# Kernel tuning notes

Measured on AMD Instinct MI355X. Metric: run time of the kernel, lower is better.

The kernel has to match this reference:

```python
import jax, jax.numpy as jnp
import numpy as np

N_E = 4096
E_DIM = 256


def setup_inputs() -> dict:
    key = jax.random.key(0)
    k1, k2 = jax.random.split(key)
    z = jax.random.normal(k1, (32, 2048, E_DIM), dtype=jnp.float32)
    # nn.Embedding weight initialized uniform(-1/n_e, 1/n_e)
    codebook = jax.random.uniform(k2, (N_E, E_DIM), dtype=jnp.float32,
                                  minval=-1.0 / N_E, maxval=1.0 / N_E)
    return {"z": z, "codebook": codebook}


def reference(z, codebook):
    # z: [B, T, e_dim], codebook: [n_e, e_dim]
    z_flat = z.reshape(-1, z.shape[-1])                      # [N, d]
    # squared euclidean distance: ||z||^2 + ||e||^2 - 2 z.e^T
    d = (jnp.sum(z_flat ** 2, axis=1, keepdims=True)
         + jnp.sum(codebook ** 2, axis=1)
         - 2.0 * jnp.einsum('nd,kd->nk', z_flat, codebook))  # [N, n_e]
    idx = jnp.argmin(d, axis=1)                              # [N]
    z_q = codebook[idx].reshape(z.shape)                     # [B, T, d]
    return z_q
```

## Files before the change

kernel.cpp:

```cpp
#include <hip/hip_runtime.h>
#include <hip/hip_fp16.h>
#include <cfloat>
#include <climits>

#define D     256
#define NE    4096
#define MT    64
#define NSPLITB 8
#define DELTA     1.5e-4f
#define CAND_CAP  131072

typedef _Float16 f16x8 __attribute__((ext_vector_type(8)));
typedef __attribute__((ext_vector_type(4))) float f32x4;

#define SYNC(n) do { \
    asm volatile("s_waitcnt vmcnt(" #n ")\n\ts_barrier" ::: "memory"); \
    __builtin_amdgcn_sched_barrier(0); \
} while (0)

__device__ __forceinline__ float np_block128_sq(const float* __restrict__ p) {
    float r[8];
    #pragma unroll
    for (int j = 0; j < 8; ++j) r[j] = __fmul_rn(p[j], p[j]);
    #pragma unroll
    for (int i = 8; i < 128; i += 8)
        #pragma unroll
        for (int j = 0; j < 8; ++j) r[j] = __fadd_rn(r[j], __fmul_rn(p[i + j], p[i + j]));
    return __fadd_rn(__fadd_rn(__fadd_rn(r[0], r[1]), __fadd_rn(r[2], r[3])),
                     __fadd_rn(__fadd_rn(r[4], r[5]), __fadd_rn(r[6], r[7])));
}
__device__ __forceinline__ float np_sumsq256(const float* __restrict__ p) {
    return __fadd_rn(np_block128_sq(p), np_block128_sq(p + 128));
}
__device__ __forceinline__ float np_einsum_dot256(const float* __restrict__ zr,
                                                  const float* __restrict__ er) {
    float v0 = 0.f, v1 = 0.f, v2 = 0.f, v3 = 0.f;
    for (int t = 0; t < 256; t += 16) {
        float4 a0 = *(const float4*)(zr + t);
        float4 a1 = *(const float4*)(zr + t + 4);
        float4 a2 = *(const float4*)(zr + t + 8);
        float4 a3 = *(const float4*)(zr + t + 12);
        float4 b0 = *(const float4*)(er + t);
        float4 b1 = *(const float4*)(er + t + 4);
        float4 b2 = *(const float4*)(er + t + 8);
        float4 b3 = *(const float4*)(er + t + 12);
        v0 = __fadd_rn(v0, __fmul_rn(a3.x, b3.x));
        v1 = __fadd_rn(v1, __fmul_rn(a3.y, b3.y));
        v2 = __fadd_rn(v2, __fmul_rn(a3.z, b3.z));
        v3 = __fadd_rn(v3, __fmul_rn(a3.w, b3.w));
        v0 = __fadd_rn(v0, __fmul_rn(a2.x, b2.x));
        v1 = __fadd_rn(v1, __fmul_rn(a2.y, b2.y));
        v2 = __fadd_rn(v2, __fmul_rn(a2.z, b2.z));
        v3 = __fadd_rn(v3, __fmul_rn(a2.w, b2.w));
        v0 = __fadd_rn(v0, __fmul_rn(a1.x, b1.x));
        v1 = __fadd_rn(v1, __fmul_rn(a1.y, b1.y));
        v2 = __fadd_rn(v2, __fmul_rn(a1.z, b1.z));
        v3 = __fadd_rn(v3, __fmul_rn(a1.w, b1.w));
        v0 = __fadd_rn(v0, __fmul_rn(a0.x, b0.x));
        v1 = __fadd_rn(v1, __fmul_rn(a0.y, b0.y));
        v2 = __fadd_rn(v2, __fmul_rn(a0.z, b0.z));
        v3 = __fadd_rn(v3, __fmul_rn(a0.w, b0.w));
    }
    return __fadd_rn(__fadd_rn(v0, v1), __fadd_rn(v2, v3));
}

__global__ void bnp_kernel(const float* __restrict__ cb, float* __restrict__ Bnp,
                           unsigned short* __restrict__ Bnpb) {
    int k = blockIdx.x * 256 + threadIdx.x;
    if (k < NE) {
        float s = np_sumsq256(cb + (size_t)k * D);
        Bnp[k] = s;
        unsigned u = __float_as_uint(s);
        Bnpb[k] = (unsigned short)((u + 0x7FFFu + ((u >> 16) & 1u)) >> 16);
    }
}

__global__ void tof16_kernel(const float* __restrict__ x,
                             unsigned short* __restrict__ y, float scale, int n4) {
    int t = blockIdx.x * 256 + threadIdx.x;
    if (t >= n4) return;
    float4 v = *(const float4*)(x + (size_t)t * 4);
    ushort4 o;
    o.x = __half_as_ushort(__float2half_rn(v.x * scale));
    o.y = __half_as_ushort(__float2half_rn(v.y * scale));
    o.z = __half_as_ushort(__float2half_rn(v.z * scale));
    o.w = __half_as_ushort(__float2half_rn(v.w * scale));
    *(ushort4*)(y + (size_t)t * 4) = o;
}

__device__ __forceinline__ void gload_lds16(const void* g, void* l) {
    __builtin_amdgcn_global_load_lds(
        (const __attribute__((address_space(1))) unsigned int*)g,
        (__attribute__((address_space(3))) unsigned int*)l, 16, 0, 0);
}

__global__ __launch_bounds__(256, 3)
void stageA_f16(const float* __restrict__ z,
                const unsigned short* __restrict__ cb2,
                const unsigned short* __restrict__ Bnpb, int* __restrict__ idxArr,
                float* __restrict__ rowMin, unsigned long long* __restrict__ rowKey,
                int* __restrict__ flagCnt, int* __restrict__ flagList) {
    __shared__ unsigned char lds[8192 + 4 * 8192];
    unsigned short* BnpL = (unsigned short*)lds;
    unsigned short* Bt = (unsigned short*)(lds + 8192);

    const int tid  = threadIdx.x;
    const int wid  = tid >> 6;
    const int lane = tid & 63;
    const int ln   = lane & 15;
    const int qd   = lane >> 4;
    const int wm   = wid & 1;
    const int wn   = wid >> 1;
    const int R0   = blockIdx.x * MT;

    #pragma unroll
    for (int i = 0; i < 2; ++i) {
        int j = tid + 256 * i;
        *(uint4*)(BnpL + j * 8) = *(const uint4*)(Bnpb + j * 8);
    }

    f16x8 fa[8][2];
    {
        const float* za = z + (size_t)(R0 + wm * 32 + ln) * 256 + qd * 8;
        #pragma unroll
        for (int kc = 0; kc < 8; ++kc)
            #pragma unroll
            for (int mt = 0; mt < 2; ++mt) {
                const float* p = za + mt * 16 * 256 + kc * 32;
                float4 a = *(const float4*)p, b = *(const float4*)(p + 4);
                f16x8 h;
                h[0] = (_Float16)a.x; h[1] = (_Float16)a.y;
                h[2] = (_Float16)a.z; h[3] = (_Float16)a.w;
                h[4] = (_Float16)b.x; h[5] = (_Float16)b.y;
                h[6] = (_Float16)b.z; h[7] = (_Float16)b.w;
                fa[kc][mt] = h;
            }
    }

    const int cA  = wid * 32 + (lane >> 2);
    const int sgA = (lane & 3) ^ ((cA >> 1) & 3);
    const unsigned short* srcA = cb2 + cA * 256 + sgA * 8;
    unsigned short* dstW = Bt + wid * 1024;
    const int boffs = ((wn * 64 + ln) << 6) + ((qd ^ ((ln >> 1) & 3)) << 4);
    const unsigned char* btb = (const unsigned char*)Bt;

    float best1[8], best2[8];
    int   bidx[8];
    #pragma unroll
    for (int i = 0; i < 8; ++i) { best1[i] = FLT_MAX; best2[i] = FLT_MAX; bidx[i] = 0; }

    #pragma unroll
    for (int s = 0; s < 3; ++s) {
        gload_lds16(srcA + s * 32, dstW + s * 4096);
        gload_lds16(srcA + s * 32 + 4096, dstW + s * 4096 + 512);
    }
    __syncthreads();

    for (int ct = 0; ct < 31; ++ct) {
        f32x4 acc[2][4];
        #pragma unroll
        for (int i = 0; i < 2; ++i)
            #pragma unroll
            for (int j = 0; j < 4; ++j) acc[i][j] = (f32x4){0.f, 0.f, 0.f, 0.f};

        #pragma unroll
        for (int kc = 0; kc < 8; ++kc) {
            SYNC(4);
            {
                const int s3k = kc + 3;
                int off = (ct + (s3k >> 3)) * 32768 + (s3k & 7) * 32;
                unsigned short* d = dstW + ((s3k & 3) << 12);
                gload_lds16(srcA + off, d);
                gload_lds16(srcA + off + 4096, d + 512);
            }
            f16x8 fb[4];
            #pragma unroll
            for (int nt = 0; nt < 4; ++nt)
                fb[nt] = *(const f16x8*)(btb + ((kc & 3) << 13) + boffs + nt * 1024);
            __builtin_amdgcn_s_setprio(1);
            #pragma unroll
            for (int mt = 0; mt < 2; ++mt)
                #pragma unroll
                for (int nt = 0; nt < 4; ++nt)
                    acc[mt][nt] = __builtin_amdgcn_mfma_f32_16x16x32_f16(
                        fa[kc][mt], fb[nt], acc[mt][nt], 0, 0, 0);
            __builtin_amdgcn_s_setprio(0);

            if (kc == 7) {
                const int C0 = ct * 128;
                #pragma unroll
                for (int nt = 0; nt < 4; ++nt) {
                    int col = C0 + wn * 64 + nt * 16 + ln;
                    float bn = __uint_as_float(((unsigned)BnpL[col]) << 16);
                    #pragma unroll
                    for (int mt = 0; mt < 2; ++mt) {
                        f32x4 a = acc[mt][nt];
                        #pragma unroll
                        for (int r = 0; r < 4; ++r) {
                            float s = fmaf(-4.8828125e-4f, a[r], bn);
                            int ii = mt * 4 + r;
                            bool lt = s < best1[ii];
                            best2[ii] = __builtin_amdgcn_fmed3f(best1[ii], best2[ii], s);
                            bidx[ii]  = lt ? col : bidx[ii];
                            best1[ii] = fminf(best1[ii], s);
                        }
                    }
                }
            }
        }
    }
    {
        const int ct = 31;
        f32x4 acc[2][4];
        #pragma unroll
        for (int i = 0; i < 2; ++i)
            #pragma unroll
            for (int j = 0; j < 4; ++j) acc[i][j] = (f32x4){0.f, 0.f, 0.f, 0.f};

        #pragma unroll
        for (int kc = 0; kc < 8; ++kc) {
            if (kc <= 5) { SYNC(4); } else if (kc == 6) { SYNC(2); } else { SYNC(0); }
            if (kc <= 4) {
                const int s3k = kc + 3;
                int off = ct * 32768 + (s3k & 7) * 32;
                unsigned short* d = dstW + ((s3k & 3) << 12);
                gload_lds16(srcA + off, d);
                gload_lds16(srcA + off + 4096, d + 512);
            }
            f16x8 fb[4];
            #pragma unroll
            for (int nt = 0; nt < 4; ++nt)
                fb[nt] = *(const f16x8*)(btb + ((kc & 3) << 13) + boffs + nt * 1024);
            __builtin_amdgcn_s_setprio(1);
            #pragma unroll
            for (int mt = 0; mt < 2; ++mt)
                #pragma unroll
                for (int nt = 0; nt < 4; ++nt)
                    acc[mt][nt] = __builtin_amdgcn_mfma_f32_16x16x32_f16(
                        fa[kc][mt], fb[nt], acc[mt][nt], 0, 0, 0);
            __builtin_amdgcn_s_setprio(0);

            if (kc == 7) {
                const int C0 = ct * 128;
                #pragma unroll
                for (int nt = 0; nt < 4; ++nt) {
                    int col = C0 + wn * 64 + nt * 16 + ln;
                    float bn = __uint_as_float(((unsigned)BnpL[col]) << 16);
                    #pragma unroll
                    for (int mt = 0; mt < 2; ++mt) {
                        f32x4 a = acc[mt][nt];
                        #pragma unroll
                        for (int r = 0; r < 4; ++r) {
                            float s = fmaf(-4.8828125e-4f, a[r], bn);
                            int ii = mt * 4 + r;
                            bool lt = s < best1[ii];
                            best2[ii] = __builtin_amdgcn_fmed3f(best1[ii], best2[ii], s);
                            bidx[ii]  = lt ? col : bidx[ii];
                            best1[ii] = fminf(best1[ii], s);
                        }
                    }
                }
            }
        }
    }

    #pragma unroll
    for (int mask = 1; mask < 16; mask <<= 1) {
        #pragma unroll
        for (int ii = 0; ii < 8; ++ii) {
            float c1 = __shfl_xor(best1[ii], mask);
            float c2 = __shfl_xor(best2[ii], mask);
            int   ci = __shfl_xor(bidx[ii], mask);
            if (c1 < best1[ii] || (c1 == best1[ii] && ci < bidx[ii])) {
                best2[ii] = fminf(best1[ii], c2);
                best1[ii] = c1; bidx[ii] = ci;
            } else {
                best2[ii] = fminf(best2[ii], c1);
            }
        }
    }
    __syncthreads();
    float* mb1 = (float*)lds;
    float* mb2 = mb1 + 128;
    int*   mix = (int*)(mb2 + 128);
    if (ln == 0) {
        #pragma unroll
        for (int mt = 0; mt < 2; ++mt)
            #pragma unroll
            for (int r = 0; r < 4; ++r) {
                int row = wm * 32 + mt * 16 + qd * 4 + r;
                mb1[row * 2 + wn] = best1[mt * 4 + r];
                mb2[row * 2 + wn] = best2[mt * 4 + r];
                mix[row * 2 + wn] = bidx[mt * 4 + r];
            }
    }
    __syncthreads();
    if (tid < MT) {
        int r = tid;
        float b1 = mb1[r * 2], b2v = mb2[r * 2]; int ix = mix[r * 2];
        float c1 = mb1[r * 2 + 1], c2 = mb2[r * 2 + 1]; int ci = mix[r * 2 + 1];
        if (c1 < b1 || (c1 == b1 && ci < ix)) { b2v = fminf(b1, c2); b1 = c1; ix = ci; }
        else b2v = fminf(b2v, c1);
        idxArr[R0 + r] = ix;
        rowMin[R0 + r] = b1;
        rowKey[R0 + r] = ~0ULL;
        if (b2v - b1 <= DELTA) {
            int p = atomicAdd(flagCnt, 1);
            flagList[p] = R0 + r;
        }
    }
}

__global__ __launch_bounds__(256, 2)
void stageB_f16(const float* __restrict__ z,
                const unsigned short* __restrict__ cb2,
                const float* __restrict__ Bnp, const float* __restrict__ rowMin,
                const int* __restrict__ flagCnt, const int* __restrict__ flagList,
                int* __restrict__ candCnt, unsigned int* __restrict__ candList) {
    __shared__ unsigned char lds[4 * 8192 + 512];
    unsigned short* Bt = (unsigned short*)lds;
    int*   frow   = (int*)(lds + 32768);
    float* rmin_l = (float*)(lds + 32768 + 256);

    const int nf = *flagCnt;
    const int R0 = blockIdx.x * MT;
    if (R0 >= nf) return;
    const int m = min(MT, nf - R0);

    const int tid  = threadIdx.x;
    const int wid  = tid >> 6;
    const int lane = tid & 63;
    const int ln   = lane & 15;
    const int qd   = lane >> 4;
    const int wn   = wid;
    const int ktBeg = blockIdx.y * (NE / NSPLITB);

    if (tid < MT) {
        int fr = flagList[R0 + min(tid, m - 1)];
        frow[tid] = fr;
        rmin_l[tid] = rowMin[fr];
    }
    __syncthreads();

    float rmv[16];
    #pragma unroll
    for (int mt = 0; mt < 4; ++mt)
        #pragma unroll
        for (int r = 0; r < 4; ++r)
            rmv[mt * 4 + r] = rmin_l[mt * 16 + qd * 4 + r];

    float bnv[4][2];
    #pragma unroll
    for (int ct = 0; ct < 4; ++ct)
        #pragma unroll
        for (int nt = 0; nt < 2; ++nt)
            bnv[ct][nt] = Bnp[ktBeg + ct * 128 + wn * 32 + nt * 16 + ln];

    f16x8 fa[8][4];
    {
        int rA[4];
        #pragma unroll
        for (int mt = 0; mt < 4; ++mt) rA[mt] = frow[mt * 16 + ln];
        #pragma unroll
        for (int kc = 0; kc < 8; ++kc)
            #pragma unroll
            for (int mt = 0; mt < 4; ++mt) {
                const float* p = z + (size_t)rA[mt] * 256 + kc * 32 + qd * 8;
                float4 a = *(const float4*)p, b = *(const float4*)(p + 4);
                f16x8 h;
                h[0] = (_Float16)a.x; h[1] = (_Float16)a.y;
                h[2] = (_Float16)a.z; h[3] = (_Float16)a.w;
                h[4] = (_Float16)b.x; h[5] = (_Float16)b.y;
                h[6] = (_Float16)b.z; h[7] = (_Float16)b.w;
                fa[kc][mt] = h;
            }
    }

    const int cA  = wid * 32 + (lane >> 2);
    const int sgA = (lane & 3) ^ ((cA >> 1) & 3);
    const unsigned short* srcA = cb2 + (size_t)(ktBeg + cA) * 256 + sgA * 8;
    unsigned short* dstW = Bt + wid * 1024;
    const int boffs = ((wn * 32 + ln) << 6) + ((qd ^ ((ln >> 1) & 3)) << 4);
    const unsigned char* btb = (const unsigned char*)Bt;

    #pragma unroll
    for (int s = 0; s < 3; ++s) {
        gload_lds16(srcA + s * 32, dstW + s * 4096);
        gload_lds16(srcA + s * 32 + 4096, dstW + s * 4096 + 512);
    }
    __syncthreads();

    unsigned long long hm0 = 0, hm1 = 0;

    #pragma unroll
    for (int ct = 0; ct < 4; ++ct) {
        f32x4 acc[4][2];
        #pragma unroll
        for (int i = 0; i < 4; ++i)
            #pragma unroll
            for (int j = 0; j < 2; ++j) acc[i][j] = (f32x4){0.f, 0.f, 0.f, 0.f};

        #pragma unroll
        for (int kc = 0; kc < 8; ++kc) {
            const int s = ct * 8 + kc;
            if (s <= 29) { SYNC(4); } else if (s == 30) { SYNC(2); } else { SYNC(0); }
            if (s <= 28) {
                const int s3 = s + 3;
                int off = (s3 >> 3) * 32768 + (s3 & 7) * 32;
                unsigned short* d = dstW + ((s3 & 3) << 12);
                gload_lds16(srcA + off, d);
                gload_lds16(srcA + off + 4096, d + 512);
            }
            f16x8 fb[2];
            #pragma unroll
            for (int nt = 0; nt < 2; ++nt)
                fb[nt] = *(const f16x8*)(btb + ((s & 3) << 13) + boffs + nt * 1024);
            __builtin_amdgcn_s_setprio(1);
            #pragma unroll
            for (int mt = 0; mt < 4; ++mt)
                #pragma unroll
                for (int nt = 0; nt < 2; ++nt)
                    acc[mt][nt] = __builtin_amdgcn_mfma_f32_16x16x32_f16(
                        fa[kc][mt], fb[nt], acc[mt][nt], 0, 0, 0);
            __builtin_amdgcn_s_setprio(0);

            if (kc == 7) {
                #pragma unroll
                for (int nt = 0; nt < 2; ++nt)
                    #pragma unroll
                    for (int mt = 0; mt < 4; ++mt) {
                        f32x4 a = acc[mt][nt];
                        #pragma unroll
                        for (int r = 0; r < 4; ++r) {
                            float sc = fmaf(-4.8828125e-4f, a[r], bnv[ct][nt]);
                            if (sc <= rmv[mt * 4 + r] + DELTA) {
                                unsigned long long bit =
                                    1ull << (((ct & 1) << 5) | (nt << 4) | (mt << 2) | r);
                                if (ct < 2) hm0 |= bit; else hm1 |= bit;
                            }
                        }
                    }
            }
        }
    }

    #pragma unroll
    for (int h = 0; h < 2; ++h) {
        unsigned long long hm = h ? hm1 : hm0;
        while (hm) {
            int b = __builtin_ctzll(hm);
            hm &= hm - 1;
            int ctb = h * 2 + (b >> 5);
            int ntb = (b >> 4) & 1, mtb = (b >> 2) & 3, rb = b & 3;
            int col = ktBeg + ctb * 128 + wn * 32 + ntb * 16 + ln;
            int row = frow[mtb * 16 + qd * 4 + rb];
            int p = atomicAdd(candCnt, 1);
            if (p < CAND_CAP)
                candList[p] = ((unsigned)row << 12) | (unsigned)col;
        }
    }
}

__global__ void stageC(const float* __restrict__ z, const float* __restrict__ cb,
                       const float* __restrict__ Bnp,
                       const int* __restrict__ candCnt,
                       const unsigned int* __restrict__ candList,
                       unsigned long long* __restrict__ rowKey) {
    int c = blockIdx.x * 256 + threadIdx.x;
    int n = min(*candCnt, CAND_CAP);
    if (c >= n) return;
    unsigned e = candList[c];
    int r = (int)(e >> 12);
    int k = (int)(e & 4095u);
    float Anp = np_sumsq256(z + (size_t)r * D);
    float C   = np_einsum_dot256(z + (size_t)r * D, cb + (size_t)k * D);
    float AB  = __fadd_rn(Anp, Bnp[k]);
    float s   = __fsub_rn(AB, __fadd_rn(C, C));
    unsigned long long key = ((unsigned long long)__float_as_uint(s) << 32) | (unsigned)k;
    atomicMin(rowKey + r, key);
}

__global__ void gather_kernel(const float* __restrict__ cb,
                              const int* __restrict__ idxArr,
                              const unsigned long long* __restrict__ rowKey,
                              float* __restrict__ out) {
    int r = blockIdx.x * 4 + (threadIdx.x >> 6);
    int l = threadIdx.x & 63;
    unsigned long long kv = rowKey[r];
    int ix = (kv != ~0ULL) ? (int)(kv & 0xFFFFFFFFull) : idxArr[r];
    *(float4*)(out + (size_t)r * D + l * 4) =
        *(const float4*)(cb + (size_t)ix * D + l * 4);
}

extern "C" void kernel_launch(void* const* d_in, const int* in_sizes, int n_in,
                              void* d_out, int out_size, void* d_ws, size_t ws_size,
                              hipStream_t stream) {
    const float* z  = (const float*)d_in[0];
    const float* cb = (const float*)d_in[1];
    float* out = (float*)d_out;
    const int nRows = in_sizes[0] / D;

    char* w = (char*)d_ws;
    unsigned short* cb2 = (unsigned short*)w;
    unsigned long long* rowKey = (unsigned long long*)(w + 2097152);
    int*   idxArr   = (int*)  (w + 2621440);
    float* rowMin   = (float*)(w + 2883584);
    int*   flagList = (int*)  (w + 3145728);
    float* Bnp      = (float*)(w + 3407872);
    unsigned short* Bnpb = (unsigned short*)(w + 3424256);
    unsigned int* candList = (unsigned int*)(w + 3432448);
    int*   flagCnt  = (int*)  (w + 3956736);
    int*   candCnt  = flagCnt + 1;

    hipMemsetAsync(flagCnt, 0, 8, stream);
    bnp_kernel<<<NE / 256, 256, 0, stream>>>(cb, Bnp, Bnpb);
    tof16_kernel<<<NE * D / 4 / 256, 256, 0, stream>>>(cb, cb2, 4096.0f, NE * D / 4);
    stageA_f16<<<nRows / MT, 256, 0, stream>>>(z, cb2, Bnpb, idxArr, rowMin,
                                               rowKey, flagCnt, flagList);
    stageB_f16<<<dim3(nRows / MT, NSPLITB), 256, 0, stream>>>(z, cb2, Bnp, rowMin,
                                                              flagCnt, flagList,
                                                              candCnt, candList);
    stageC<<<CAND_CAP / 256, 256, 0, stream>>>(z, cb, Bnp, candCnt, candList, rowKey);
    gather_kernel<<<nRows / 4, 256, 0, stream>>>(cb, idxArr, rowKey, out);
}
```

Before: 438.4 us.

## Shrink stage A row tile and give each wave its own codebook slice

Stage A now processes 32 rows per block instead of 64. Each of the four waves owns a private 32-column slice of the codebook tile, which it streams into its own LDS region. This replaces the block-wide barriers in the K loop with per-wave vmcnt waits only, and the final reduction merges four per-wave candidates instead of two. The cost is that every codebook byte is now loaded for half as many rows, which doubles codebook traffic through L2, and each wave issues fewer MFMAs per B fragment load.

```diff
diff --git a/kernel.cpp b/kernel.cpp
--- a/kernel.cpp
+++ b/kernel.cpp
@@ -5,13 +5,19 @@
 
 #define D     256
 #define NE    4096
-#define MT    64
+#define MTA   32
+#define MTB   64
 #define NSPLITB 8
 #define DELTA     1.5e-4f
 #define CAND_CAP  131072
 
 typedef _Float16 f16x8 __attribute__((ext_vector_type(8)));
 typedef __attribute__((ext_vector_type(4))) float f32x4;
+
+#define WAITV(n) do { \
+    asm volatile("s_waitcnt vmcnt(" #n ")" ::: "memory"); \
+    __builtin_amdgcn_sched_barrier(0); \
+} while (0)
 
 #define SYNC(n) do { \
     asm volatile("s_waitcnt vmcnt(" #n ")\n\ts_barrier" ::: "memory"); \
@@ -102,16 +108,13 @@
                 int* __restrict__ flagCnt, int* __restrict__ flagList) {
     __shared__ unsigned char lds[8192 + 4 * 8192];
     unsigned short* BnpL = (unsigned short*)lds;
-    unsigned short* Bt = (unsigned short*)(lds + 8192);
 
     const int tid  = threadIdx.x;
     const int wid  = tid >> 6;
     const int lane = tid & 63;
     const int ln   = lane & 15;
     const int qd   = lane >> 4;
-    const int wm   = wid & 1;
-    const int wn   = wid >> 1;
-    const int R0   = blockIdx.x * MT;
+    const int R0   = blockIdx.x * MTA;
 
     #pragma unroll
     for (int i = 0; i < 2; ++i) {
@@ -121,7 +124,7 @@
 
     f16x8 fa[8][2];
     {
-        const float* za = z + (size_t)(R0 + wm * 32 + ln) * 256 + qd * 8;
+        const float* za = z + (size_t)(R0 + ln) * 256 + qd * 8;
         #pragma unroll
         for (int kc = 0; kc < 8; ++kc)
             #pragma unroll
@@ -137,60 +140,61 @@
             }
     }
 
-    const int cA  = wid * 32 + (lane >> 2);
-    const int sgA = (lane & 3) ^ ((cA >> 1) & 3);
-    const unsigned short* srcA = cb2 + cA * 256 + sgA * 8;
-    unsigned short* dstW = Bt + wid * 1024;
-    const int boffs = ((wn * 64 + ln) << 6) + ((qd ^ ((ln >> 1) & 3)) << 4);
-    const unsigned char* btb = (const unsigned char*)Bt;
+    const int cL  = lane >> 2;
+    const int sgA = (lane & 3) ^ ((cL >> 1) & 3);
+    const unsigned short* srcA = cb2 + (wid * 32 + cL) * 256 + sgA * 8;
+    unsigned short* dstW = (unsigned short*)(lds + 8192) + wid * 4096;
+    const unsigned char* btb = lds + 8192 + wid * 8192;
+    const int boffs = (ln << 6) + ((qd ^ ((ln >> 1) & 3)) << 4);
 
     float best1[8], best2[8];
     int   bidx[8];
     #pragma unroll
     for (int i = 0; i < 8; ++i) { best1[i] = FLT_MAX; best2[i] = FLT_MAX; bidx[i] = 0; }
 
+    __syncthreads();
+
     #pragma unroll
     for (int s = 0; s < 3; ++s) {
-        gload_lds16(srcA + s * 32, dstW + s * 4096);
-        gload_lds16(srcA + s * 32 + 4096, dstW + s * 4096 + 512);
-    }
-    __syncthreads();
+        gload_lds16(srcA + s * 32, dstW + s * 1024);
+        gload_lds16(srcA + s * 32 + 4096, dstW + s * 1024 + 512);
+    }
 
     for (int ct = 0; ct < 31; ++ct) {
-        f32x4 acc[2][4];
+        f32x4 acc[2][2];
         #pragma unroll
         for (int i = 0; i < 2; ++i)
             #pragma unroll
-            for (int j = 0; j < 4; ++j) acc[i][j] = (f32x4){0.f, 0.f, 0.f, 0.f};
+            for (int j = 0; j < 2; ++j) acc[i][j] = (f32x4){0.f, 0.f, 0.f, 0.f};
 
         #pragma unroll
         for (int kc = 0; kc < 8; ++kc) {
-            SYNC(4);
+            WAITV(4);
             {
                 const int s3k = kc + 3;
                 int off = (ct + (s3k >> 3)) * 32768 + (s3k & 7) * 32;
-                unsigned short* d = dstW + ((s3k & 3) << 12);
+                unsigned short* d = dstW + ((s3k & 3) << 10);
                 gload_lds16(srcA + off, d);
                 gload_lds16(srcA + off + 4096, d + 512);
             }
-            f16x8 fb[4];
-            #pragma unroll
-            for (int nt = 0; nt < 4; ++nt)
-                fb[nt] = *(const f16x8*)(btb + ((kc & 3) << 13) + boffs + nt * 1024);
+            f16x8 fb[2];
+            #pragma unroll
+            for (int nt = 0; nt < 2; ++nt)
+                fb[nt] = *(const f16x8*)(btb + ((kc & 3) << 11) + boffs + nt * 1024);
             __builtin_amdgcn_s_setprio(1);
             #pragma unroll
             for (int mt = 0; mt < 2; ++mt)
                 #pragma unroll
-                for (int nt = 0; nt < 4; ++nt)
+                for (int nt = 0; nt < 2; ++nt)
                     acc[mt][nt] = __builtin_amdgcn_mfma_f32_16x16x32_f16(
                         fa[kc][mt], fb[nt], acc[mt][nt], 0, 0, 0);
             __builtin_amdgcn_s_setprio(0);
 
             if (kc == 7) {
-                const int C0 = ct * 128;
+                const int C0 = ct * 128 + wid * 32;
                 #pragma unroll
-                for (int nt = 0; nt < 4; ++nt) {
-                    int col = C0 + wn * 64 + nt * 16 + ln;
+                for (int nt = 0; nt < 2; ++nt) {
+                    int col = C0 + nt * 16 + ln;
                     float bn = __uint_as_float(((unsigned)BnpL[col]) << 16);
                     #pragma unroll
                     for (int mt = 0; mt < 2; ++mt) {
@@ -211,40 +215,40 @@
     }
     {
         const int ct = 31;
-        f32x4 acc[2][4];
+        f32x4 acc[2][2];
         #pragma unroll
         for (int i = 0; i < 2; ++i)
             #pragma unroll
-            for (int j = 0; j < 4; ++j) acc[i][j] = (f32x4){0.f, 0.f, 0.f, 0.f};
+            for (int j = 0; j < 2; ++j) acc[i][j] = (f32x4){0.f, 0.f, 0.f, 0.f};
 
         #pragma unroll
         for (int kc = 0; kc < 8; ++kc) {
-            if (kc <= 5) { SYNC(4); } else if (kc == 6) { SYNC(2); } else { SYNC(0); }
+            if (kc <= 5) { WAITV(4); } else if (kc == 6) { WAITV(2); } else { WAITV(0); }
             if (kc <= 4) {
                 const int s3k = kc + 3;
                 int off = ct * 32768 + (s3k & 7) * 32;
-                unsigned short* d = dstW + ((s3k & 3) << 12);
+                unsigned short* d = dstW + ((s3k & 3) << 10);
                 gload_lds16(srcA + off, d);
                 gload_lds16(srcA + off + 4096, d + 512);
             }
-            f16x8 fb[4];
-            #pragma unroll
-            for (int nt = 0; nt < 4; ++nt)
-                fb[nt] = *(const f16x8*)(btb + ((kc & 3) << 13) + boffs + nt * 1024);
+            f16x8 fb[2];
+            #pragma unroll
+            for (int nt = 0; nt < 2; ++nt)
+                fb[nt] = *(const f16x8*)(btb + ((kc & 3) << 11) + boffs + nt * 1024);
             __builtin_amdgcn_s_setprio(1);
             #pragma unroll
             for (int mt = 0; mt < 2; ++mt)
                 #pragma unroll
-                for (int nt = 0; nt < 4; ++nt)
+                for (int nt = 0; nt < 2; ++nt)
                     acc[mt][nt] = __builtin_amdgcn_mfma_f32_16x16x32_f16(
                         fa[kc][mt], fb[nt], acc[mt][nt], 0, 0, 0);
             __builtin_amdgcn_s_setprio(0);
 
             if (kc == 7) {
-                const int C0 = ct * 128;
+                const int C0 = ct * 128 + wid * 32;
                 #pragma unroll
-                for (int nt = 0; nt < 4; ++nt) {
-                    int col = C0 + wn * 64 + nt * 16 + ln;
+                for (int nt = 0; nt < 2; ++nt) {
+                    int col = C0 + nt * 16 + ln;
                     float bn = __uint_as_float(((unsigned)BnpL[col]) << 16);
                     #pragma unroll
                     for (int mt = 0; mt < 2; ++mt) {
@@ -288,19 +292,22 @@
         for (int mt = 0; mt < 2; ++mt)
             #pragma unroll
             for (int r = 0; r < 4; ++r) {
-                int row = wm * 32 + mt * 16 + qd * 4 + r;
-                mb1[row * 2 + wn] = best1[mt * 4 + r];
-                mb2[row * 2 + wn] = best2[mt * 4 + r];
-                mix[row * 2 + wn] = bidx[mt * 4 + r];
+                int row = mt * 16 + qd * 4 + r;
+                mb1[row * 4 + wid] = best1[mt * 4 + r];
+                mb2[row * 4 + wid] = best2[mt * 4 + r];
+                mix[row * 4 + wid] = bidx[mt * 4 + r];
             }
     }
     __syncthreads();
-    if (tid < MT) {
+    if (tid < MTA) {
         int r = tid;
-        float b1 = mb1[r * 2], b2v = mb2[r * 2]; int ix = mix[r * 2];
-        float c1 = mb1[r * 2 + 1], c2 = mb2[r * 2 + 1]; int ci = mix[r * 2 + 1];
-        if (c1 < b1 || (c1 == b1 && ci < ix)) { b2v = fminf(b1, c2); b1 = c1; ix = ci; }
-        else b2v = fminf(b2v, c1);
+        float b1 = mb1[r * 4], b2v = mb2[r * 4]; int ix = mix[r * 4];
+        #pragma unroll
+        for (int w = 1; w < 4; ++w) {
+            float c1 = mb1[r * 4 + w], c2 = mb2[r * 4 + w]; int ci = mix[r * 4 + w];
+            if (c1 < b1 || (c1 == b1 && ci < ix)) { b2v = fminf(b1, c2); b1 = c1; ix = ci; }
+            else b2v = fminf(b2v, c1);
+        }
         idxArr[R0 + r] = ix;
         rowMin[R0 + r] = b1;
         rowKey[R0 + r] = ~0ULL;
@@ -323,9 +330,9 @@
     float* rmin_l = (float*)(lds + 32768 + 256);
 
     const int nf = *flagCnt;
-    const int R0 = blockIdx.x * MT;
+    const int R0 = blockIdx.x * MTB;
     if (R0 >= nf) return;
-    const int m = min(MT, nf - R0);
+    const int m = min(MTB, nf - R0);
 
     const int tid  = threadIdx.x;
     const int wid  = tid >> 6;
@@ -335,7 +342,7 @@
     const int wn   = wid;
     const int ktBeg = blockIdx.y * (NE / NSPLITB);
 
-    if (tid < MT) {
+    if (tid < MTB) {
         int fr = flagList[R0 + min(tid, m - 1)];
         frow[tid] = fr;
         rmin_l[tid] = rowMin[fr];
@@ -515,11 +522,11 @@
     hipMemsetAsync(flagCnt, 0, 8, stream);
     bnp_kernel<<<NE / 256, 256, 0, stream>>>(cb, Bnp, Bnpb);
     tof16_kernel<<<NE * D / 4 / 256, 256, 0, stream>>>(cb, cb2, 4096.0f, NE * D / 4);
-    stageA_f16<<<nRows / MT, 256, 0, stream>>>(z, cb2, Bnpb, idxArr, rowMin,
-                                               rowKey, flagCnt, flagList);
-    stageB_f16<<<dim3(nRows / MT, NSPLITB), 256, 0, stream>>>(z, cb2, Bnp, rowMin,
-                                                              flagCnt, flagList,
-                                                              candCnt, candList);
+    stageA_f16<<<nRows / MTA, 256, 0, stream>>>(z, cb2, Bnpb, idxArr, rowMin,
+                                                rowKey, flagCnt, flagList);
+    stageB_f16<<<dim3(nRows / MTB, NSPLITB), 256, 0, stream>>>(z, cb2, Bnp, rowMin,
+                                                               flagCnt, flagList,
+                                                               candCnt, candList);
     stageC<<<CAND_CAP / 256, 256, 0, stream>>>(z, cb, Bnp, candCnt, candList, rowKey);
     gather_kernel<<<nRows / 4, 256, 0, stream>>>(cb, idxArr, rowKey, out);
 }
```

After: 509.9 us. +16.3%, slower.

## Double-buffer B fragments in stage A and halve stage B codebook splits

Applied to the files above, without the earlier changes.

In the first-pass kernel, the B-operand fragments for the next k-chunk are read from LDS before the current chunk's MFMAs run, and the wait count is tightened accordingly. This is meant to hide LDS read latency behind matrix math, at the cost of extra registers. Separately, the flagged-row rescoring kernel now splits the codebook into 4 parts instead of 8, so each block covers 8 column tiles. That gives fewer blocks with longer loops and halves the redundant reloads of the A operand.

```diff
diff --git a/kernel.cpp b/kernel.cpp
--- a/kernel.cpp
+++ b/kernel.cpp
@@ -6,7 +6,7 @@
 #define D     256
 #define NE    4096
 #define MT    64
-#define NSPLITB 8
+#define NSPLITB 4
 #define DELTA     1.5e-4f
 #define CAND_CAP  131072
 
@@ -149,12 +149,18 @@
     #pragma unroll
     for (int i = 0; i < 8; ++i) { best1[i] = FLT_MAX; best2[i] = FLT_MAX; bidx[i] = 0; }
 
+    __syncthreads();
+
     #pragma unroll
     for (int s = 0; s < 3; ++s) {
         gload_lds16(srcA + s * 32, dstW + s * 4096);
         gload_lds16(srcA + s * 32 + 4096, dstW + s * 4096 + 512);
     }
-    __syncthreads();
+    SYNC(4);
+    f16x8 fbc[4];
+    #pragma unroll
+    for (int nt = 0; nt < 4; ++nt)
+        fbc[nt] = *(const f16x8*)(btb + boffs + nt * 1024);
 
     for (int ct = 0; ct < 31; ++ct) {
         f32x4 acc[2][4];
@@ -165,7 +171,7 @@
 
         #pragma unroll
         for (int kc = 0; kc < 8; ++kc) {
-            SYNC(4);
+            SYNC(2);
             {
                 const int s3k = kc + 3;
                 int off = (ct + (s3k >> 3)) * 32768 + (s3k & 7) * 32;
@@ -173,17 +179,17 @@
                 gload_lds16(srcA + off, d);
                 gload_lds16(srcA + off + 4096, d + 512);
             }
-            f16x8 fb[4];
+            f16x8 fbn[4];
             #pragma unroll
             for (int nt = 0; nt < 4; ++nt)
-                fb[nt] = *(const f16x8*)(btb + ((kc & 3) << 13) + boffs + nt * 1024);
+                fbn[nt] = *(const f16x8*)(btb + (((kc + 1) & 3) << 13) + boffs + nt * 1024);
             __builtin_amdgcn_s_setprio(1);
             #pragma unroll
             for (int mt = 0; mt < 2; ++mt)
                 #pragma unroll
                 for (int nt = 0; nt < 4; ++nt)
                     acc[mt][nt] = __builtin_amdgcn_mfma_f32_16x16x32_f16(
-                        fa[kc][mt], fb[nt], acc[mt][nt], 0, 0, 0);
+                        fa[kc][mt], fbc[nt], acc[mt][nt], 0, 0, 0);
             __builtin_amdgcn_s_setprio(0);
 
             if (kc == 7) {
@@ -207,6 +213,8 @@
                     }
                 }
             }
+            #pragma unroll
+            for (int nt = 0; nt < 4; ++nt) fbc[nt] = fbn[nt];
         }
     }
     {
@@ -219,7 +227,7 @@
 
         #pragma unroll
         for (int kc = 0; kc < 8; ++kc) {
-            if (kc <= 5) { SYNC(4); } else if (kc == 6) { SYNC(2); } else { SYNC(0); }
+            if (kc <= 5) { SYNC(2); } else if (kc == 6) { SYNC(0); }
             if (kc <= 4) {
                 const int s3k = kc + 3;
                 int off = ct * 32768 + (s3k & 7) * 32;
@@ -227,17 +235,19 @@
                 gload_lds16(srcA + off, d);
                 gload_lds16(srcA + off + 4096, d + 512);
             }
-            f16x8 fb[4];
-            #pragma unroll
-            for (int nt = 0; nt < 4; ++nt)
-                fb[nt] = *(const f16x8*)(btb + ((kc & 3) << 13) + boffs + nt * 1024);
+            f16x8 fbn[4];
+            if (kc <= 6) {
+                #pragma unroll
+                for (int nt = 0; nt < 4; ++nt)
+                    fbn[nt] = *(const f16x8*)(btb + (((kc + 1) & 3) << 13) + boffs + nt * 1024);
+            }
             __builtin_amdgcn_s_setprio(1);
             #pragma unroll
             for (int mt = 0; mt < 2; ++mt)
                 #pragma unroll
                 for (int nt = 0; nt < 4; ++nt)
                     acc[mt][nt] = __builtin_amdgcn_mfma_f32_16x16x32_f16(
-                        fa[kc][mt], fb[nt], acc[mt][nt], 0, 0, 0);
+                        fa[kc][mt], fbc[nt], acc[mt][nt], 0, 0, 0);
             __builtin_amdgcn_s_setprio(0);
 
             if (kc == 7) {
@@ -260,6 +270,9 @@
                         }
                     }
                 }
+            } else {
+                #pragma unroll
+                for (int nt = 0; nt < 4; ++nt) fbc[nt] = fbn[nt];
             }
         }
     }
@@ -349,9 +362,9 @@
         for (int r = 0; r < 4; ++r)
             rmv[mt * 4 + r] = rmin_l[mt * 16 + qd * 4 + r];
 
-    float bnv[4][2];
-    #pragma unroll
-    for (int ct = 0; ct < 4; ++ct)
+    float bnv[8][2];
+    #pragma unroll
+    for (int ct = 0; ct < 8; ++ct)
         #pragma unroll
         for (int nt = 0; nt < 2; ++nt)
             bnv[ct][nt] = Bnp[ktBeg + ct * 128 + wn * 32 + nt * 16 + ln];
@@ -390,10 +403,10 @@
     }
     __syncthreads();
 
-    unsigned long long hm0 = 0, hm1 = 0;
-
-    #pragma unroll
-    for (int ct = 0; ct < 4; ++ct) {
+    unsigned long long hm0 = 0, hm1 = 0, hm2 = 0, hm3 = 0;
+
+    #pragma unroll
+    for (int ct = 0; ct < 8; ++ct) {
         f32x4 acc[4][2];
         #pragma unroll
         for (int i = 0; i < 4; ++i)
@@ -403,8 +416,8 @@
         #pragma unroll
         for (int kc = 0; kc < 8; ++kc) {
             const int s = ct * 8 + kc;
-            if (s <= 29) { SYNC(4); } else if (s == 30) { SYNC(2); } else { SYNC(0); }
-            if (s <= 28) {
+            if (s <= 61) { SYNC(4); } else if (s == 62) { SYNC(2); } else { SYNC(0); }
+            if (s <= 60) {
                 const int s3 = s + 3;
                 int off = (s3 >> 3) * 32768 + (s3 & 7) * 32;
                 unsigned short* d = dstW + ((s3 & 3) << 12);
@@ -436,7 +449,10 @@
                             if (sc <= rmv[mt * 4 + r] + DELTA) {
                                 unsigned long long bit =
                                     1ull << (((ct & 1) << 5) | (nt << 4) | (mt << 2) | r);
-                                if (ct < 2) hm0 |= bit; else hm1 |= bit;
+                                if (ct < 2)      hm0 |= bit;
+                                else if (ct < 4) hm1 |= bit;
+                                else if (ct < 6) hm2 |= bit;
+                                else             hm3 |= bit;
                             }
                         }
                     }
@@ -445,8 +461,8 @@
     }
 
     #pragma unroll
-    for (int h = 0; h < 2; ++h) {
-        unsigned long long hm = h ? hm1 : hm0;
+    for (int h = 0; h < 4; ++h) {
+        unsigned long long hm = (h == 0) ? hm0 : (h == 1) ? hm1 : (h == 2) ? hm2 : hm3;
         while (hm) {
             int b = __builtin_ctzll(hm);
             hm &= hm - 1;
```

After: 504.3 us. 1.15x slower.
